# Optimization experiments

Measured on AMD Instinct MI355X. Metric: run time of the kernel, lower is better.

## Reference

```python
import jax, jax.numpy as jnp
import numpy as np

B, S, H = 256, 196, 1024  # batch, image_size**2, hidden_size


def _linear_init(key, fan_in, fan_out):
    kw, kb = jax.random.split(key)
    lim = 1.0 / np.sqrt(fan_in)
    W = jax.random.uniform(kw, (fan_in, fan_out), jnp.float32, -lim, lim)
    b = jax.random.uniform(kb, (fan_out,), jnp.float32, -lim, lim)
    return W, b


def setup_inputs() -> dict:
    key = jax.random.key(0)
    ks = jax.random.split(key, 7)
    v = jax.random.normal(ks[0], (B, S, H), jnp.float32)
    h = jax.random.normal(ks[1], (B, H), jnp.float32)
    W_fc, b_fc = _linear_init(ks[2], H, 2 * H)
    W_v, b_v = _linear_init(ks[3], H, H)
    W_h, b_h = _linear_init(ks[4], H, H)
    W_s, b_s = _linear_init(ks[5], H, H)
    W_z, b_z = _linear_init(ks[6], H, 1)
    return {"v": v, "h": h, "W_fc": W_fc, "b_fc": b_fc, "W_v": W_v, "b_v": b_v,
            "W_h": W_h, "b_h": b_h, "W_s": W_s, "b_s": b_s, "W_z": W_z, "b_z": b_z}


def reference(v, h, W_fc, b_fc, W_v, b_v, W_h, b_h, W_s, b_s, W_z, b_z):
    # Dropout is identity in eval mode.
    hs = jnp.tanh(h[:, None, :] @ W_fc + b_fc)          # (B, 1, 2H)
    h1, s = hs[..., :H], hs[..., H:]                    # each (B, 1, H)
    _v = v @ W_v + b_v                                  # (B, S, H)
    _h = h1 @ W_h + b_h                                 # (B, 1, H)
    _s = s @ W_s + b_s                                  # (B, 1, H)
    z = jnp.tanh(jnp.concatenate([_v, _s], axis=1) + _h)  # (B, S+1, H)
    z = (z @ W_z + b_z)[..., 0]                         # (B, S+1)
    a = jax.nn.softmax(z, axis=1)                       # (B, S+1)
    vc = jnp.concatenate([v, s], axis=1)                # (B, S+1, H)
    c = jnp.sum(a[:, :, None] * vc, axis=1)             # (B, H)
    return a, c
```

## Files before the change

### kernel.cpp

```cpp
#include <hip/hip_runtime.h>
#include <hip/hip_bf16.h>
#include <cstdint>
#include <cstddef>

#define Bb  256
#define Ss  196
#define Hh  1024
#define SP1 197
#define Mm  50176

typedef float  f32x4 __attribute__((ext_vector_type(4)));
typedef short  s16x8 __attribute__((ext_vector_type(8)));
typedef unsigned short u16;
typedef unsigned short u16x8 __attribute__((ext_vector_type(8)));

__device__ __forceinline__ u16 f2b(float f) {
  __hip_bfloat16 b = __float2bfloat16(f);
  u16 r; __builtin_memcpy(&r, &b, 2); return r;
}
__device__ __forceinline__ float b2f(u16 u) {
  return __uint_as_float(((unsigned)u) << 16);
}
__device__ __forceinline__ float ftanh(float x) {
  float ax = fabsf(x);
  float t = __expf(-2.f * ax);
  float r = (1.f - t) * __builtin_amdgcn_rcpf(1.f + t);
  return copysignf(r, x);
}
__device__ __forceinline__ void gload16(const u16* g, u16* l) {
  __builtin_amdgcn_global_load_lds(
      (const __attribute__((address_space(1))) unsigned int*)(const void*)g,
      (__attribute__((address_space(3))) unsigned int*)(void*)l, 16, 0, 0);
}

__global__ __launch_bounds__(256) void k_transpose_cvt(const float* __restrict__ Wv,
                                                       u16* __restrict__ WvT) {
  __shared__ float t[64][65];
  int k0 = (blockIdx.x & 15) * 64;
  int n0 = (blockIdx.x >> 4) * 64;
  int tid = threadIdx.x;
#pragma unroll
  for (int i = 0; i < 16; ++i) {
    int idx = i * 256 + tid;
    int r = idx >> 6, c = idx & 63;
    t[r][c] = Wv[(size_t)(k0 + r) * Hh + n0 + c];
  }
  __syncthreads();
#pragma unroll
  for (int i = 0; i < 16; ++i) {
    int idx = i * 256 + tid;
    int r = idx >> 6, c = idx & 63;
    WvT[(size_t)(n0 + r) * Hh + ((k0 + c) ^ ((r & 7) << 3))] = f2b(t[c][r]);
  }
}

__global__ __launch_bounds__(256) void k_cvtV(const float* __restrict__ V,
                                              u16* __restrict__ Vb) {
  int c = blockIdx.x * 256 + threadIdx.x;
  int m = c >> 7;
  int k8 = (c & 127) << 3;
  f32x4 a = *(const f32x4*)(V + (size_t)m * Hh + k8);
  f32x4 b = *(const f32x4*)(V + (size_t)m * Hh + k8 + 4);
  u16x8 w;
  w[0] = f2b(a.x); w[1] = f2b(a.y); w[2] = f2b(a.z); w[3] = f2b(a.w);
  w[4] = f2b(b.x); w[5] = f2b(b.y); w[6] = f2b(b.z); w[7] = f2b(b.w);
  *(u16x8*)(Vb + (size_t)m * Hh + (k8 ^ ((m & 7) << 3))) = w;
}

__device__ __forceinline__ void small_gemm_core(int bid, int nct,
    const float* __restrict__ X, int ldx,
    const float* __restrict__ W, int ldw,
    const float* __restrict__ bias,
    float* __restrict__ Y, int ldy, int act) {
  __shared__ float xs[4][16][64];
  int tid = threadIdx.x, lane = tid & 63, w = tid >> 6;
  int ct = bid % nct, bt = bid / nct;
  int col = ct * 64 + lane;
  float acc[16];
#pragma unroll
  for (int b = 0; b < 16; ++b) acc[b] = 0.f;
  int xr = lane >> 2, xc = (lane & 3) * 16;
  for (int kc = 0; kc < 4; ++kc) {
    int kb = w * 256 + kc * 64;
#pragma unroll
    for (int q = 0; q < 4; ++q)
      *(f32x4*)&xs[w][xr][xc + q * 4] =
          *(const f32x4*)&X[(size_t)(bt * 16 + xr) * ldx + kb + xc + q * 4];
    for (int kl = 0; kl < 64; kl += 4) {
      float w0 = W[(size_t)(kb + kl + 0) * ldw + col];
      float w1 = W[(size_t)(kb + kl + 1) * ldw + col];
      float w2 = W[(size_t)(kb + kl + 2) * ldw + col];
      float w3 = W[(size_t)(kb + kl + 3) * ldw + col];
#pragma unroll
      for (int b = 0; b < 16; ++b) {
        f32x4 x = *(const f32x4*)&xs[w][b][kl];
        acc[b] += x.x * w0 + x.y * w1 + x.z * w2 + x.w * w3;
      }
    }
  }
#pragma unroll
  for (int b = 0; b < 16; ++b) xs[w][b][lane] = acc[b];
  __syncthreads();
#pragma unroll
  for (int q = 0; q < 4; ++q) {
    int b = w * 4 + q;
    float s = xs[0][b][lane] + xs[1][b][lane] + xs[2][b][lane] + xs[3][b][lane]
            + bias[col];
    if (act) s = ftanh(s);
    Y[(size_t)(bt * 16 + b) * ldy + col] = s;
  }
}

__global__ __launch_bounds__(256) void k_fc(const float* __restrict__ h,
                                            const float* __restrict__ Wfc,
                                            const float* __restrict__ bfc,
                                            float* __restrict__ hs) {
  small_gemm_core(blockIdx.x, 32, h, Hh, Wfc, 2048, bfc, hs, 2048, 1);
}

__global__ __launch_bounds__(256) void k_dual(const float* __restrict__ hs,
                                              const float* __restrict__ Wh,
                                              const float* __restrict__ bh,
                                              const float* __restrict__ Ws_,
                                              const float* __restrict__ bs_,
                                              float* __restrict__ hhp,
                                              float* __restrict__ svp) {
  int bid = blockIdx.x;
  int sel = bid >= 256;
  small_gemm_core(bid - (sel << 8), 16,
                  sel ? hs + 1024 : hs, 2048,
                  sel ? Ws_ : Wh, Hh,
                  sel ? bs_ : bh,
                  sel ? svp : hhp, Hh, 0);
}

#define BK 64
template<int PRE>
__global__ __launch_bounds__(256, PRE ? 4 : 3)
void k_big(const float* __restrict__ V, const u16* __restrict__ Vb,
           const u16* __restrict__ WvT, const float* __restrict__ bv,
           const float* __restrict__ hh, const float* __restrict__ Wz,
           float* __restrict__ zpart) {
  constexpr int LDA_ = PRE ? 64 : 72;
  __shared__ __align__(16) u16 As[128 * LDA_];
  __shared__ __align__(16) u16 Bs[128 * 64];
  __shared__ float wz_s[128], bv_s[128], hh_s[2][128];
  __shared__ float zred[4][64];

  int bid = blockIdx.x;
  int lin = (bid & 7) * 392 + (bid >> 3);
  int mt = lin >> 3, nt = lin & 7;
  int row0 = mt * 128, n0 = nt * 128;

  int tid = threadIdx.x;
  int lane = tid & 63, wid = tid >> 6;
  int wm = wid >> 1, wn = wid & 1;

  int b0 = row0 / Ss;
  int rsplit = (b0 + 1) * Ss - row0;
  int b1 = (rsplit < 128) ? b0 + 1 : b0;
  if (tid < 128) {
    wz_s[tid] = Wz[n0 + tid];
    bv_s[tid] = bv[n0 + tid];
    hh_s[0][tid] = hh[(size_t)b0 * Hh + n0 + tid];
    hh_s[1][tid] = hh[(size_t)b1 * Hh + n0 + tid];
  }

  f32x4 acc[4][4];
  f32x4 zz = {0.f, 0.f, 0.f, 0.f};
#pragma unroll
  for (int m = 0; m < 4; ++m)
#pragma unroll
    for (int n = 0; n < 4; ++n) acc[m][n] = zz;

  int srow = lane >> 3, scol = (lane & 7) * 8;
  int bxor = (lane & 7) << 3;

  int arow = tid >> 3, acol8 = (tid & 7) * 8;
  const float* Ap = V + (size_t)(row0 + arow) * Hh + acol8;
  f32x4 av[8];
  if constexpr (!PRE) {
#pragma unroll
    for (int j = 0; j < 4; ++j) {
      av[2 * j]     = *(const f32x4*)(Ap + (size_t)j * 32 * Hh);
      av[2 * j + 1] = *(const f32x4*)(Ap + (size_t)j * 32 * Hh + 4);
    }
  }

  for (int kt = 0; kt < 16; ++kt) {
    int k0 = kt * BK;
    __syncthreads();
#pragma unroll
    for (int i = 0; i < 4; ++i) {
      int r = wid * 32 + i * 8;
      gload16(WvT + (size_t)(n0 + r + srow) * Hh + k0 + scol, &Bs[r * 64]);
    }
    if constexpr (PRE) {
#pragma unroll
      for (int i = 0; i < 4; ++i) {
        int r = wid * 32 + i * 8;
        gload16(Vb + (size_t)(row0 + r + srow) * Hh + k0 + scol, &As[r * 64]);
      }
    } else {
#pragma unroll
      for (int j = 0; j < 4; ++j) {
        u16x8 w;
        w[0] = f2b(av[2 * j].x);     w[1] = f2b(av[2 * j].y);
        w[2] = f2b(av[2 * j].z);     w[3] = f2b(av[2 * j].w);
        w[4] = f2b(av[2 * j + 1].x); w[5] = f2b(av[2 * j + 1].y);
        w[6] = f2b(av[2 * j + 1].z); w[7] = f2b(av[2 * j + 1].w);
        *(u16x8*)&As[(j * 32 + arow) * LDA_ + acol8] = w;
      }
      if (kt < 15) {
#pragma unroll
        for (int j = 0; j < 4; ++j) {
          av[2 * j]     = *(const f32x4*)(Ap + (size_t)j * 32 * Hh + k0 + BK);
          av[2 * j + 1] = *(const f32x4*)(Ap + (size_t)j * 32 * Hh + k0 + BK + 4);
        }
      }
    }
    __syncthreads();
#pragma unroll
    for (int ks = 0; ks < 2; ++ks) {
      int kk = ks * 32 + (lane >> 4) * 8;
      s16x8 afr[4], bfr[4];
#pragma unroll
      for (int m = 0; m < 4; ++m) {
        int r = wm * 64 + m * 16 + (lane & 15);
        afr[m] = *(const s16x8*)&As[r * LDA_ + (PRE ? (kk ^ bxor) : kk)];
      }
#pragma unroll
      for (int n = 0; n < 4; ++n) {
        int r = wn * 64 + n * 16 + (lane & 15);
        bfr[n] = *(const s16x8*)&Bs[r * 64 + (kk ^ bxor)];
      }
#pragma unroll
      for (int m = 0; m < 4; ++m)
#pragma unroll
        for (int n = 0; n < 4; ++n)
          acc[m][n] = __builtin_amdgcn_mfma_f32_16x16x32_bf16(afr[m], bfr[n], acc[m][n], 0, 0, 0);
    }
  }

  int cl = lane & 15, rg = lane >> 4;
  float pz[4][4];
#pragma unroll
  for (int m = 0; m < 4; ++m)
#pragma unroll
    for (int j = 0; j < 4; ++j) pz[m][j] = 0.f;
#pragma unroll
  for (int n = 0; n < 4; ++n) {
    int col = wn * 64 + n * 16 + cl;
    float wzv = wz_s[col], bvv = bv_s[col];
    float h0 = hh_s[0][col], h1 = hh_s[1][col];
#pragma unroll
    for (int m = 0; m < 4; ++m)
#pragma unroll
      for (int j = 0; j < 4; ++j) {
        int r = wm * 64 + m * 16 + rg * 4 + j;
        float hv = (r >= rsplit) ? h1 : h0;
        pz[m][j] += wzv * ftanh(acc[m][n][j] + bvv + hv);
      }
  }
#pragma unroll
  for (int m = 0; m < 4; ++m)
#pragma unroll
    for (int j = 0; j < 4; ++j) {
      float vv = pz[m][j];
      vv += __shfl_xor(vv, 1); vv += __shfl_xor(vv, 2);
      vv += __shfl_xor(vv, 4); vv += __shfl_xor(vv, 8);
      pz[m][j] = vv;
    }
  if (cl == 0) {
#pragma unroll
    for (int m = 0; m < 4; ++m)
#pragma unroll
      for (int j = 0; j < 4; ++j)
        zred[wid][m * 16 + rg * 4 + j] = pz[m][j];
  }
  __syncthreads();
  if (tid < 128) {
    int hhalf = tid >> 6, lr = tid & 63;
    zpart[(size_t)nt * Mm + row0 + tid] =
        zred[hhalf * 2][lr] + zred[hhalf * 2 + 1][lr];
  }
}

__global__ __launch_bounds__(256) void k_softmax(const float* __restrict__ zpart,
                                                 const float* __restrict__ sv,
                                                 const float* __restrict__ hhp,
                                                 const float* __restrict__ Wz,
                                                 const float* __restrict__ bz,
                                                 float* __restrict__ outA) {
  int b = blockIdx.x, tid = threadIdx.x;
  int wid = tid >> 6, lane = tid & 63;
  __shared__ float redm[4], reds[4];
  __shared__ float zSsh;
  {
    int j0 = tid * 4;
    f32x4 s4 = *(const f32x4*)&sv[(size_t)b * Hh + j0];
    f32x4 h4 = *(const f32x4*)&hhp[(size_t)b * Hh + j0];
    f32x4 w4 = *(const f32x4*)&Wz[j0];
    float p = w4.x * ftanh(s4.x + h4.x) + w4.y * ftanh(s4.y + h4.y)
            + w4.z * ftanh(s4.z + h4.z) + w4.w * ftanh(s4.w + h4.w);
#pragma unroll
    for (int d = 1; d < 64; d <<= 1) p += __shfl_xor(p, d);
    if (lane == 0) redm[wid] = p;
    __syncthreads();
    if (tid == 0) zSsh = redm[0] + redm[1] + redm[2] + redm[3] + bz[0];
    __syncthreads();
  }
  float z = -1e30f;
  if (tid < Ss) {
    float s = 0.f;
#pragma unroll
    for (int nt = 0; nt < 8; ++nt) s += zpart[(size_t)nt * Mm + (size_t)b * Ss + tid];
    z = s + bz[0];
  } else if (tid == Ss) {
    z = zSsh;
  }
  float m = z;
#pragma unroll
  for (int d = 1; d < 64; d <<= 1) m = fmaxf(m, __shfl_xor(m, d));
  if (lane == 0) redm[wid] = m;
  __syncthreads();
  m = fmaxf(fmaxf(redm[0], redm[1]), fmaxf(redm[2], redm[3]));
  float e = (tid <= Ss) ? expf(z - m) : 0.f;
  float s = e;
#pragma unroll
  for (int d = 1; d < 64; d <<= 1) s += __shfl_xor(s, d);
  if (lane == 0) reds[wid] = s;
  __syncthreads();
  s = reds[0] + reds[1] + reds[2] + reds[3];
  if (tid <= Ss) outA[(size_t)b * SP1 + tid] = e / s;
}

template<int PRE>
__global__ __launch_bounds__(256) void k_ctx(const float* __restrict__ V,
                                             const u16* __restrict__ Vb,
                                             const float* __restrict__ hs,
                                             const float* __restrict__ A,
                                             float* __restrict__ outC) {
  int b = blockIdx.x >> 2;
  int col = (blockIdx.x & 3) * 256 + threadIdx.x;
  __shared__ float a_s[SP1];
  if (threadIdx.x < SP1) a_s[threadIdx.x] = A[(size_t)b * SP1 + threadIdx.x];
  __syncthreads();
  float acc = a_s[Ss] * hs[(size_t)b * 2048 + 1024 + col];
  if constexpr (PRE) {
    size_t m0 = (size_t)b * Ss;
#pragma unroll 4
    for (int t = 0; t < Ss; ++t) {
      size_t m = m0 + t;
      acc += a_s[t] * b2f(Vb[m * Hh + (col ^ (((int)m & 7) << 3))]);
    }
  } else {
    const float* vb = V + (size_t)b * Ss * Hh + col;
#pragma unroll 4
    for (int t = 0; t < Ss; ++t) acc += a_s[t] * vb[(size_t)t * Hh];
  }
  outC[(size_t)b * Hh + col] = acc;
}

extern "C" void kernel_launch(void* const* d_in, const int* in_sizes, int n_in,
                              void* d_out, int out_size, void* d_ws, size_t ws_size,
                              hipStream_t stream) {
  const float* v   = (const float*)d_in[0];
  const float* h   = (const float*)d_in[1];
  const float* Wfc = (const float*)d_in[2];
  const float* bfc = (const float*)d_in[3];
  const float* Wv  = (const float*)d_in[4];
  const float* bv  = (const float*)d_in[5];
  const float* Wh  = (const float*)d_in[6];
  const float* bh  = (const float*)d_in[7];
  const float* Ws  = (const float*)d_in[8];
  const float* bs  = (const float*)d_in[9];
  const float* Wz  = (const float*)d_in[10];
  const float* bz  = (const float*)d_in[11];
  float* out  = (float*)d_out;
  float* outA = out;
  float* outC = out + (size_t)Bb * SP1;

  float* ws  = (float*)d_ws;
  float* hs  = ws;
  float* hh  = hs + 524288;
  float* sv  = hh + 262144;
  float* zp  = sv + 262144;
  u16*  WvT  = (u16*)(zp + 401408);
  u16*  Vb   = (u16*)((char*)(void*)WvT + 2097152);

  bool pre = ws_size >= 110657536ull;

  k_transpose_cvt<<<256, 256, 0, stream>>>(Wv, WvT);
  k_fc<<<512, 256, 0, stream>>>(h, Wfc, bfc, hs);
  k_dual<<<512, 256, 0, stream>>>(hs, Wh, bh, Ws, bs, hh, sv);
  if (pre) {
    k_cvtV<<<25088, 256, 0, stream>>>(v, Vb);
    k_big<1><<<3136, 256, 0, stream>>>(v, Vb, WvT, bv, hh, Wz, zp);
  } else {
    k_big<0><<<3136, 256, 0, stream>>>(v, Vb, WvT, bv, hh, Wz, zp);
  }
  k_softmax<<<256, 256, 0, stream>>>(zp, sv, hh, Wz, bz, outA);
  if (pre) k_ctx<1><<<1024, 256, 0, stream>>>(v, Vb, hs, outA, outC);
  else     k_ctx<0><<<1024, 256, 0, stream>>>(v, Vb, hs, outA, outC);
}
```

Measured before the change: 300.4 us.

## Fuse preprocessing kernels and double-buffer LDS tiles in pre-converted GEMM path

Three prep launches (V-to-bf16 conversion, Wv transpose/convert, fc GEMM) become one kernel that splits work by block index, with V conversion done by a grid-stride loop over 2048 blocks. The PRE variant of the main GEMM now double-buffers the A and B LDS tiles, issuing async global-to-LDS loads for the next k-step before computing the current one, with one barrier per iteration instead of two. The goal is to cut launch gaps and hide load latency behind MFMA work. In exchange LDS use doubles and the occupancy hint drops from 4 to 2 blocks per CU.

```diff
diff --git a/kernel.cpp b/kernel.cpp
--- a/kernel.cpp
+++ b/kernel.cpp
@@ -33,11 +33,26 @@
       (__attribute__((address_space(3))) unsigned int*)(void*)l, 16, 0, 0);
 }
 
-__global__ __launch_bounds__(256) void k_transpose_cvt(const float* __restrict__ Wv,
-                                                       u16* __restrict__ WvT) {
-  __shared__ float t[64][65];
-  int k0 = (blockIdx.x & 15) * 64;
-  int n0 = (blockIdx.x >> 4) * 64;
+__device__ __forceinline__ void cvtV_core(int bid, const float* __restrict__ V,
+                                          u16* __restrict__ Vb) {
+  for (int c = bid * 256 + (int)threadIdx.x; c < Mm * 128; c += 2048 * 256) {
+    int m = c >> 7;
+    int k8 = (c & 127) << 3;
+    f32x4 a = *(const f32x4*)(V + (size_t)m * Hh + k8);
+    f32x4 b = *(const f32x4*)(V + (size_t)m * Hh + k8 + 4);
+    u16x8 w;
+    w[0] = f2b(a.x); w[1] = f2b(a.y); w[2] = f2b(a.z); w[3] = f2b(a.w);
+    w[4] = f2b(b.x); w[5] = f2b(b.y); w[6] = f2b(b.z); w[7] = f2b(b.w);
+    *(u16x8*)(Vb + (size_t)m * Hh + (k8 ^ ((m & 7) << 3))) = w;
+  }
+}
+
+__device__ __forceinline__ void transpose_core(int bid, float* sm,
+                                               const float* __restrict__ Wv,
+                                               u16* __restrict__ WvT) {
+  float (*t)[65] = (float(*)[65])sm;
+  int k0 = (bid & 15) * 64;
+  int n0 = (bid >> 4) * 64;
   int tid = threadIdx.x;
 #pragma unroll
   for (int i = 0; i < 16; ++i) {
@@ -54,25 +69,11 @@
   }
 }
 
-__global__ __launch_bounds__(256) void k_cvtV(const float* __restrict__ V,
-                                              u16* __restrict__ Vb) {
-  int c = blockIdx.x * 256 + threadIdx.x;
-  int m = c >> 7;
-  int k8 = (c & 127) << 3;
-  f32x4 a = *(const f32x4*)(V + (size_t)m * Hh + k8);
-  f32x4 b = *(const f32x4*)(V + (size_t)m * Hh + k8 + 4);
-  u16x8 w;
-  w[0] = f2b(a.x); w[1] = f2b(a.y); w[2] = f2b(a.z); w[3] = f2b(a.w);
-  w[4] = f2b(b.x); w[5] = f2b(b.y); w[6] = f2b(b.z); w[7] = f2b(b.w);
-  *(u16x8*)(Vb + (size_t)m * Hh + (k8 ^ ((m & 7) << 3))) = w;
-}
-
-__device__ __forceinline__ void small_gemm_core(int bid, int nct,
+__device__ __forceinline__ void small_gemm_core(int bid, int nct, float* sm,
     const float* __restrict__ X, int ldx,
     const float* __restrict__ W, int ldw,
     const float* __restrict__ bias,
     float* __restrict__ Y, int ldy, int act) {
-  __shared__ float xs[4][16][64];
   int tid = threadIdx.x, lane = tid & 63, w = tid >> 6;
   int ct = bid % nct, bt = bid / nct;
   int col = ct * 64 + lane;
@@ -84,7 +85,7 @@
     int kb = w * 256 + kc * 64;
 #pragma unroll
     for (int q = 0; q < 4; ++q)
-      *(f32x4*)&xs[w][xr][xc + q * 4] =
+      *(f32x4*)&sm[(w * 16 + xr) * 64 + xc + q * 4] =
           *(const f32x4*)&X[(size_t)(bt * 16 + xr) * ldx + kb + xc + q * 4];
     for (int kl = 0; kl < 64; kl += 4) {
       float w0 = W[(size_t)(kb + kl + 0) * ldw + col];
@@ -93,29 +94,43 @@
       float w3 = W[(size_t)(kb + kl + 3) * ldw + col];
 #pragma unroll
       for (int b = 0; b < 16; ++b) {
-        f32x4 x = *(const f32x4*)&xs[w][b][kl];
+        f32x4 x = *(const f32x4*)&sm[(w * 16 + b) * 64 + kl];
         acc[b] += x.x * w0 + x.y * w1 + x.z * w2 + x.w * w3;
       }
     }
   }
 #pragma unroll
-  for (int b = 0; b < 16; ++b) xs[w][b][lane] = acc[b];
+  for (int b = 0; b < 16; ++b) sm[(w * 16 + b) * 64 + lane] = acc[b];
   __syncthreads();
 #pragma unroll
   for (int q = 0; q < 4; ++q) {
     int b = w * 4 + q;
-    float s = xs[0][b][lane] + xs[1][b][lane] + xs[2][b][lane] + xs[3][b][lane]
+    float s = sm[(0 * 16 + b) * 64 + lane] + sm[(1 * 16 + b) * 64 + lane]
+            + sm[(2 * 16 + b) * 64 + lane] + sm[(3 * 16 + b) * 64 + lane]
             + bias[col];
     if (act) s = ftanh(s);
     Y[(size_t)(bt * 16 + b) * ldy + col] = s;
   }
 }
 
-__global__ __launch_bounds__(256) void k_fc(const float* __restrict__ h,
-                                            const float* __restrict__ Wfc,
-                                            const float* __restrict__ bfc,
-                                            float* __restrict__ hs) {
-  small_gemm_core(blockIdx.x, 32, h, Hh, Wfc, 2048, bfc, hs, 2048, 1);
+__global__ __launch_bounds__(256) void k_pre(const float* __restrict__ v,
+                                             u16* __restrict__ Vb,
+                                             const float* __restrict__ Wv,
+                                             u16* __restrict__ WvT,
+                                             const float* __restrict__ h,
+                                             const float* __restrict__ Wfc,
+                                             const float* __restrict__ bfc,
+                                             float* __restrict__ hs,
+                                             int pre) {
+  __shared__ __align__(16) float sm[64 * 65];
+  int bid = blockIdx.x;
+  if (bid < 2048) {
+    if (pre) cvtV_core(bid, v, Vb);
+  } else if (bid < 2304) {
+    transpose_core(bid - 2048, sm, Wv, WvT);
+  } else {
+    small_gemm_core(bid - 2304, 32, sm, h, Hh, Wfc, 2048, bfc, hs, 2048, 1);
+  }
 }
 
 __global__ __launch_bounds__(256) void k_dual(const float* __restrict__ hs,
@@ -125,9 +140,10 @@
                                               const float* __restrict__ bs_,
                                               float* __restrict__ hhp,
                                               float* __restrict__ svp) {
+  __shared__ __align__(16) float sm[4 * 16 * 64];
   int bid = blockIdx.x;
   int sel = bid >= 256;
-  small_gemm_core(bid - (sel << 8), 16,
+  small_gemm_core(bid - (sel << 8), 16, sm,
                   sel ? hs + 1024 : hs, 2048,
                   sel ? Ws_ : Wh, Hh,
                   sel ? bs_ : bh,
@@ -136,14 +152,15 @@
 
 #define BK 64
 template<int PRE>
-__global__ __launch_bounds__(256, PRE ? 4 : 3)
+__global__ __launch_bounds__(256, PRE ? 2 : 3)
 void k_big(const float* __restrict__ V, const u16* __restrict__ Vb,
            const u16* __restrict__ WvT, const float* __restrict__ bv,
            const float* __restrict__ hh, const float* __restrict__ Wz,
            float* __restrict__ zpart) {
   constexpr int LDA_ = PRE ? 64 : 72;
-  __shared__ __align__(16) u16 As[128 * LDA_];
-  __shared__ __align__(16) u16 Bs[128 * 64];
+  constexpr int NBUF = PRE ? 2 : 1;
+  __shared__ __align__(16) u16 As[NBUF][128 * LDA_];
+  __shared__ __align__(16) u16 Bs[NBUF][128 * 64];
   __shared__ float wz_s[128], bv_s[128], hh_s[2][128];
   __shared__ float zred[4][64];
 
@@ -176,6 +193,20 @@
   int srow = lane >> 3, scol = (lane & 7) * 8;
   int bxor = (lane & 7) << 3;
 
+  auto stage = [&](int kt, int buf) {
+    int k0 = kt * BK;
+#pragma unroll
+    for (int i = 0; i < 4; ++i) {
+      int r = wid * 32 + i * 8;
+      gload16(WvT + (size_t)(n0 + r + srow) * Hh + k0 + scol, &Bs[buf][r * 64]);
+    }
+#pragma unroll
+    for (int i = 0; i < 4; ++i) {
+      int r = wid * 32 + i * 8;
+      gload16(Vb + (size_t)(row0 + r + srow) * Hh + k0 + scol, &As[buf][r * 64]);
+    }
+  };
+
   int arow = tid >> 3, acol8 = (tid & 7) * 8;
   const float* Ap = V + (size_t)(row0 + arow) * Hh + acol8;
   f32x4 av[8];
@@ -187,21 +218,23 @@
     }
   }
 
+  if constexpr (PRE) {
+    stage(0, 0);
+    __syncthreads();
+  }
+  int cur = 0;
+
   for (int kt = 0; kt < 16; ++kt) {
-    int k0 = kt * BK;
-    __syncthreads();
-#pragma unroll
-    for (int i = 0; i < 4; ++i) {
-      int r = wid * 32 + i * 8;
-      gload16(WvT + (size_t)(n0 + r + srow) * Hh + k0 + scol, &Bs[r * 64]);
-    }
     if constexpr (PRE) {
+      if (kt < 15) stage(kt + 1, cur ^ 1);
+    } else {
+      int k0 = kt * BK;
+      __syncthreads();
 #pragma unroll
       for (int i = 0; i < 4; ++i) {
         int r = wid * 32 + i * 8;
-        gload16(Vb + (size_t)(row0 + r + srow) * Hh + k0 + scol, &As[r * 64]);
-      }
-    } else {
+        gload16(WvT + (size_t)(n0 + r + srow) * Hh + k0 + scol, &Bs[0][r * 64]);
+      }
 #pragma unroll
       for (int j = 0; j < 4; ++j) {
         u16x8 w;
@@ -209,7 +242,7 @@
         w[2] = f2b(av[2 * j].z);     w[3] = f2b(av[2 * j].w);
         w[4] = f2b(av[2 * j + 1].x); w[5] = f2b(av[2 * j + 1].y);
         w[6] = f2b(av[2 * j + 1].z); w[7] = f2b(av[2 * j + 1].w);
-        *(u16x8*)&As[(j * 32 + arow) * LDA_ + acol8] = w;
+        *(u16x8*)&As[0][(j * 32 + arow) * LDA_ + acol8] = w;
       }
       if (kt < 15) {
 #pragma unroll
@@ -218,8 +251,8 @@
           av[2 * j + 1] = *(const f32x4*)(Ap + (size_t)j * 32 * Hh + k0 + BK + 4);
         }
       }
-    }
-    __syncthreads();
+      __syncthreads();
+    }
 #pragma unroll
     for (int ks = 0; ks < 2; ++ks) {
       int kk = ks * 32 + (lane >> 4) * 8;
@@ -227,18 +260,22 @@
 #pragma unroll
       for (int m = 0; m < 4; ++m) {
         int r = wm * 64 + m * 16 + (lane & 15);
-        afr[m] = *(const s16x8*)&As[r * LDA_ + (PRE ? (kk ^ bxor) : kk)];
+        afr[m] = *(const s16x8*)&As[cur][r * LDA_ + (PRE ? (kk ^ bxor) : kk)];
       }
 #pragma unroll
       for (int n = 0; n < 4; ++n) {
         int r = wn * 64 + n * 16 + (lane & 15);
-        bfr[n] = *(const s16x8*)&Bs[r * 64 + (kk ^ bxor)];
+        bfr[n] = *(const s16x8*)&Bs[cur][r * 64 + (kk ^ bxor)];
       }
 #pragma unroll
       for (int m = 0; m < 4; ++m)
 #pragma unroll
         for (int n = 0; n < 4; ++n)
           acc[m][n] = __builtin_amdgcn_mfma_f32_16x16x32_bf16(afr[m], bfr[n], acc[m][n], 0, 0, 0);
+    }
+    if constexpr (PRE) {
+      __syncthreads();
+      cur ^= 1;
     }
   }
 
@@ -391,15 +428,10 @@
 
   bool pre = ws_size >= 110657536ull;
 
-  k_transpose_cvt<<<256, 256, 0, stream>>>(Wv, WvT);
-  k_fc<<<512, 256, 0, stream>>>(h, Wfc, bfc, hs);
+  k_pre<<<2816, 256, 0, stream>>>(v, Vb, Wv, WvT, h, Wfc, bfc, hs, (int)pre);
   k_dual<<<512, 256, 0, stream>>>(hs, Wh, bh, Ws, bs, hh, sv);
-  if (pre) {
-    k_cvtV<<<25088, 256, 0, stream>>>(v, Vb);
-    k_big<1><<<3136, 256, 0, stream>>>(v, Vb, WvT, bv, hh, Wz, zp);
-  } else {
-    k_big<0><<<3136, 256, 0, stream>>>(v, Vb, WvT, bv, hh, Wz, zp);
-  }
+  if (pre) k_big<1><<<3136, 256, 0, stream>>>(v, Vb, WvT, bv, hh, Wz, zp);
+  else     k_big<0><<<3136, 256, 0, stream>>>(v, Vb, WvT, bv, hh, Wz, zp);
   k_softmax<<<256, 256, 0, stream>>>(zp, sv, hh, Wz, bz, outA);
   if (pre) k_ctx<1><<<1024, 256, 0, stream>>>(v, Vb, hs, outA, outC);
   else     k_ctx<0><<<1024, 256, 0, stream>>>(v, Vb, hs, outA, outC);
```

Result: slower. 311.5 us (+3.7%).
